# Performance work log

Hardware: AMD Instinct MI355X
Metric: run time of the kernel (lower is better)

Reference implementation:

```python
import jax, jax.numpy as jnp
import numpy as np

HEAD_SIZE = 128  # matches init head_size; original scales by global head_size**-0.5


def setup_inputs() -> dict:
    key = jax.random.key(0)
    k1, k2, k3, k4 = jax.random.split(key, 4)
    B, T, C, D = 16, 2048, 1024, HEAD_SIZE
    x = jax.random.normal(k1, (B, T, C), dtype=jnp.float32)
    # torch Linear weight is [out,in]; store transposed so forward is x @ W
    Wq = jax.random.normal(k2, (C, D), dtype=jnp.float32) * (C ** -0.5)
    Wk = jax.random.normal(k3, (C, D), dtype=jnp.float32) * (C ** -0.5)
    Wv = jax.random.normal(k4, (C, D), dtype=jnp.float32) * (C ** -0.5)
    return {"x": x, "Wq": Wq, "Wk": Wk, "Wv": Wv}


def reference(x, Wq, Wk, Wv):
    # x: [B,T,C]; projections -> [B,T,D]
    q = x @ Wq
    k = x @ Wk
    v = x @ Wv
    T = x.shape[1]
    scale = HEAD_SIZE ** -0.5
    # scores: [B,T,T]
    wei = jnp.einsum("btd,bsd->bts", q, k) * scale
    causal = jnp.tril(jnp.ones((T, T), dtype=bool))  # tril buffer
    wei = jnp.where(causal, wei, -jnp.inf)
    wei = jax.nn.softmax(wei, axis=-1)
    # dropout is identity in eval mode (deterministic reference)
    return wei @ v  # [B,T,D]
```

## Files before the change

### kernel.cpp

```cpp
#include <hip/hip_runtime.h>
#include <hip/hip_bf16.h>

typedef short bf16x8 __attribute__((ext_vector_type(8)));
typedef float f32x4 __attribute__((ext_vector_type(4)));
typedef unsigned short u16x4 __attribute__((ext_vector_type(4)));

#define B_ 16
#define T_ 2048
#define C_ 1024
#define D_ 128
#define M_ (B_ * T_)

static __device__ __forceinline__ unsigned short f2bf(float f) {
    unsigned int u = __builtin_bit_cast(unsigned int, f);
    unsigned int r = (u + 0x7fffu + ((u >> 16) & 1u)) >> 16;
    return (unsigned short)r;
}

static __device__ __forceinline__ void gll16(const unsigned short* g, unsigned short* l) {
    __builtin_amdgcn_global_load_lds(
        (const __attribute__((address_space(1))) void*)g,
        (__attribute__((address_space(3))) void*)l, 16, 0, 0);
}

__global__ void cvt_kernel(const float* __restrict__ x, unsigned short* __restrict__ xb) {
    int idx = blockIdx.x * 256 + threadIdx.x;
#pragma unroll
    for (int it = 0; it < 4; ++it, idx += 1048576) {
        const int row = idx >> 7;
        const int g   = idx & 127;
        const int gs  = (g & ~7) | ((g & 7) ^ (row & 7));
        const float* src = x + (size_t)row * C_ + g * 8;
        float4 v0 = *(const float4*)src;
        float4 v1 = *(const float4*)(src + 4);
        bf16x8 h;
        h[0] = (short)f2bf(v0.x); h[1] = (short)f2bf(v0.y);
        h[2] = (short)f2bf(v0.z); h[3] = (short)f2bf(v0.w);
        h[4] = (short)f2bf(v1.x); h[5] = (short)f2bf(v1.y);
        h[6] = (short)f2bf(v1.z); h[7] = (short)f2bf(v1.w);
        *(bf16x8*)&xb[(size_t)row * C_ + gs * 8] = h;
    }
}

#define TPAD 133

__global__ void wt_kernel(const float* __restrict__ Wq, const float* __restrict__ Wk,
                          const float* __restrict__ Wv, unsigned short* __restrict__ Wt) {
    __shared__ float Tl[64 * TPAD];
    const int o  = blockIdx.x >> 4;
    const int k0 = (blockIdx.x & 15) * 64;
    const float* W = (o == 0) ? Wq : (o == 1) ? Wk : Wv;
    const int tid = threadIdx.x;

    const int kr = tid >> 5;
    const int n4 = (tid & 31) * 4;
#pragma unroll
    for (int j = 0; j < 8; ++j) {
        float4 v = *(const float4*)(W + (size_t)(k0 + kr + j * 8) * 128 + n4);
        *(float4*)&Tl[(kr + j * 8) * TPAD + n4] = v;
    }
    __syncthreads();

    const int nb = tid >> 3;
    const int kg = (tid & 7) * 8;
#pragma unroll
    for (int j = 0; j < 4; ++j) {
        const int nn = nb + j * 32;
        const int kk = kg ^ ((nn & 7) * 8);
        bf16x8 v;
#pragma unroll
        for (int e = 0; e < 8; ++e)
            v[e] = (short)f2bf(Tl[(kk + e) * TPAD + nn]);
        *(bf16x8*)&Wt[((size_t)o * 128 + nn) * 1024 + k0 + kg] = v;
    }
}

__launch_bounds__(256, 3)
__global__ void qkv_kernel(const unsigned short* __restrict__ xb, const unsigned short* __restrict__ Wt,
                           unsigned short* __restrict__ Q, unsigned short* __restrict__ K,
                           unsigned short* __restrict__ Vt) {
    __shared__ unsigned short Alds[128 * 64];
    __shared__ unsigned short Blds[128 * 64];

    const int tid  = threadIdx.x;
    const int lane = tid & 63;
    const int w    = tid >> 6;
    const int wr   = w >> 1;
    const int wc   = w & 1;
    const int lr   = lane & 15;
    const int lk   = lane >> 4;

    const int nt = blockIdx.x >> 8;
    const int mt = blockIdx.x & 255;
    const int m0 = mt * 128;
    const int n0 = nt * 128;

    const int srow = tid >> 3;
    const int sg   = (tid & 7) * 8;

    f32x4 acc[4][4] = {};

    for (int t = 0; t < 16; ++t) {
        const int k0 = t * 64;
#pragma unroll
        for (int j = 0; j < 4; ++j) {
            gll16(xb + (size_t)(m0 + j * 32 + srow) * C_ + k0 + sg,
                  &Alds[(j * 32 + w * 8) * 64]);
            gll16(Wt + (size_t)(n0 + j * 32 + srow) * C_ + k0 + sg,
                  &Blds[(j * 32 + w * 8) * 64]);
        }
        __syncthreads();

#pragma unroll
        for (int kk = 0; kk < 2; ++kk) {
            bf16x8 a[4], b[4];
#pragma unroll
            for (int rb = 0; rb < 4; ++rb) {
                const int row = wr * 64 + rb * 16 + lr;
                a[rb] = *(bf16x8*)&Alds[row * 64 + ((kk * 32 + lk * 8) ^ ((row & 7) * 8))];
            }
#pragma unroll
            for (int nb = 0; nb < 4; ++nb) {
                const int row = wc * 64 + nb * 16 + lr;
                b[nb] = *(bf16x8*)&Blds[row * 64 + ((kk * 32 + lk * 8) ^ ((row & 7) * 8))];
            }
#pragma unroll
            for (int rb = 0; rb < 4; ++rb)
#pragma unroll
                for (int nb = 0; nb < 4; ++nb)
                    acc[rb][nb] = __builtin_amdgcn_mfma_f32_16x16x32_bf16(a[rb], b[nb], acc[rb][nb], 0, 0, 0);
        }
        __syncthreads();
    }

    const float qscale = 0.08838834764831845f;
    const int b  = m0 / T_;
    const int t0 = m0 % T_;
#pragma unroll
    for (int rb = 0; rb < 4; ++rb) {
#pragma unroll
        for (int nb = 0; nb < 4; ++nb) {
            const int row0 = wr * 64 + rb * 16 + lk * 4;
            const int d    = wc * 64 + nb * 16 + lr;
            f32x4 a = acc[rb][nb];
            if (nt == 0) {
#pragma unroll
                for (int r = 0; r < 4; ++r)
                    Q[(size_t)(m0 + row0 + r) * D_ + d] = f2bf(a[r] * qscale);
            } else if (nt == 1) {
#pragma unroll
                for (int r = 0; r < 4; ++r)
                    K[(size_t)(m0 + row0 + r) * D_ + d] = f2bf(a[r]);
            } else {
                u16x4 pv;
#pragma unroll
                for (int r = 0; r < 4; ++r) pv[r] = f2bf(a[r]);
                *(u16x4*)&Vt[((size_t)b * D_ + d) * T_ + t0 + row0] = pv;
            }
        }
    }
}

#define KSTR 132
#define VSTR 68
#define PSTR 68

__launch_bounds__(256, 2)
__global__ void attn_kernel(const unsigned short* __restrict__ Q, const unsigned short* __restrict__ K,
                            const unsigned short* __restrict__ Vt, float* __restrict__ out) {
    __shared__ unsigned short Klds[2][64 * KSTR];
    __shared__ unsigned short Vlds[2][128 * VSTR];
    __shared__ unsigned short Plds[4][16 * PSTR];

    const int tid  = threadIdx.x;
    const int lane = tid & 63;
    const int w    = tid >> 6;
    const int lr   = lane & 15;
    const int lk   = lane >> 4;

    int bid = blockIdx.x;
    int batch, qt;
    if (bid < 256) { batch = bid >> 4; qt = bid & 15; }
    else           { bid -= 256; batch = bid >> 4; qt = 31 - (bid & 15); }

    const unsigned short* Qb = Q  + (size_t)batch * T_ * D_;
    const unsigned short* Kb = K  + (size_t)batch * T_ * D_;
    const unsigned short* Vb = Vt + (size_t)batch * D_ * T_;
    float* outb = out + (size_t)batch * T_ * D_;

    const int kxr = tid >> 4;
    const int kxc = (tid & 15) * 8;
    const int vxr = tid >> 3;
    const int vxc = (tid & 7) * 8;

    bf16x8 kr[4], vr[4];
    auto kv_load = [&](int kvt) {
        const int kv0 = kvt * 64;
#pragma unroll
        for (int j = 0; j < 4; ++j)
            kr[j] = *(const bf16x8*)(Kb + (size_t)(kv0 + kxr + j * 16) * D_ + kxc);
#pragma unroll
        for (int j = 0; j < 4; ++j)
            vr[j] = *(const bf16x8*)(Vb + (size_t)(vxr + j * 32) * T_ + kv0 + vxc);
    };
    auto kv_write = [&](int buf) {
#pragma unroll
        for (int j = 0; j < 4; ++j)
            *(bf16x8*)&Klds[buf][(kxr + j * 16) * KSTR + kxc] = kr[j];
#pragma unroll
        for (int j = 0; j < 4; ++j)
            *(bf16x8*)&Vlds[buf][(vxr + j * 32) * VSTR + vxc] = vr[j];
    };

    const int qw = qt * 64 + w * 16;

    bf16x8 qf[4];
#pragma unroll
    for (int c = 0; c < 4; ++c)
        qf[c] = *(const bf16x8*)(Qb + (size_t)(qw + lr) * D_ + lk * 8 + c * 32);

    f32x4 o_acc[8] = {};
    float mrun[4] = {-1e30f, -1e30f, -1e30f, -1e30f};
    float lrun[4] = {0.f, 0.f, 0.f, 0.f};

    kv_load(0);
    kv_write(0);

    for (int kvt = 0; kvt <= qt; ++kvt) {
        const int cur = kvt & 1;
        __syncthreads();
        if (kvt < qt) kv_load(kvt + 1);

        f32x4 s[4];
#pragma unroll
        for (int nb = 0; nb < 4; ++nb) {
            f32x4 a = {};
#pragma unroll
            for (int c = 0; c < 4; ++c) {
                bf16x8 kf = *(bf16x8*)&Klds[cur][(nb * 16 + lr) * KSTR + lk * 8 + c * 32];
                a = __builtin_amdgcn_mfma_f32_16x16x32_bf16(qf[c], kf, a, 0, 0, 0);
            }
            s[nb] = a;
        }

        if (kvt == qt) {
#pragma unroll
            for (int nb = 0; nb < 4; ++nb)
#pragma unroll
                for (int r = 0; r < 4; ++r) {
                    int qg = qw + lk * 4 + r;
                    int kg = kvt * 64 + nb * 16 + lr;
                    if (kg > qg) s[nb][r] = -1e30f;
                }
        }

        float scale_[4];
#pragma unroll
        for (int r = 0; r < 4; ++r) {
            float mx = fmaxf(fmaxf(s[0][r], s[1][r]), fmaxf(s[2][r], s[3][r]));
            mx = fmaxf(mx, __shfl_xor(mx, 1));
            mx = fmaxf(mx, __shfl_xor(mx, 2));
            mx = fmaxf(mx, __shfl_xor(mx, 4));
            mx = fmaxf(mx, __shfl_xor(mx, 8));
            float mnew = fmaxf(mrun[r], mx);
            scale_[r]  = __expf(mrun[r] - mnew);
            mrun[r]    = mnew;
            lrun[r]   *= scale_[r];
        }
#pragma unroll
        for (int db = 0; db < 8; ++db)
#pragma unroll
            for (int r = 0; r < 4; ++r) o_acc[db][r] *= scale_[r];

#pragma unroll
        for (int nb = 0; nb < 4; ++nb)
#pragma unroll
            for (int r = 0; r < 4; ++r) {
                float p = __expf(s[nb][r] - mrun[r]);
                lrun[r] += p;
                Plds[w][(lk * 4 + r) * PSTR + nb * 16 + lr] = f2bf(p);
            }
        asm volatile("s_waitcnt lgkmcnt(0)" ::: "memory");
        __builtin_amdgcn_sched_barrier(0);

        bf16x8 pa[2];
#pragma unroll
        for (int c = 0; c < 2; ++c)
            pa[c] = *(bf16x8*)&Plds[w][lr * PSTR + lk * 8 + c * 32];
#pragma unroll
        for (int db = 0; db < 8; ++db) {
            f32x4 oo = o_acc[db];
#pragma unroll
            for (int c = 0; c < 2; ++c) {
                bf16x8 vf = *(bf16x8*)&Vlds[cur][(db * 16 + lr) * VSTR + lk * 8 + c * 32];
                oo = __builtin_amdgcn_mfma_f32_16x16x32_bf16(pa[c], vf, oo, 0, 0, 0);
            }
            o_acc[db] = oo;
        }

        if (kvt < qt) kv_write(cur ^ 1);
    }

#pragma unroll
    for (int r = 0; r < 4; ++r) {
        float sgm = lrun[r];
        sgm += __shfl_xor(sgm, 1);
        sgm += __shfl_xor(sgm, 2);
        sgm += __shfl_xor(sgm, 4);
        sgm += __shfl_xor(sgm, 8);
        lrun[r] = 1.0f / sgm;
    }
#pragma unroll
    for (int db = 0; db < 8; ++db)
#pragma unroll
        for (int r = 0; r < 4; ++r)
            outb[(size_t)(qw + lk * 4 + r) * D_ + db * 16 + lr] = o_acc[db][r] * lrun[r];
}

extern "C" void kernel_launch(void* const* d_in, const int* in_sizes, int n_in,
                              void* d_out, int out_size, void* d_ws, size_t ws_size,
                              hipStream_t stream) {
    const float* x  = (const float*)d_in[0];
    const float* Wq = (const float*)d_in[1];
    const float* Wk = (const float*)d_in[2];
    const float* Wv = (const float*)d_in[3];

    unsigned short* xb  = (unsigned short*)d_ws;
    unsigned short* Wt  = (unsigned short*)((char*)d_ws + (64u << 20));
    unsigned short* Qw  = (unsigned short*)((char*)d_ws + (65u << 20));
    unsigned short* Kw  = Qw + (size_t)M_ * D_;
    unsigned short* Vtw = Kw + (size_t)M_ * D_;

    hipLaunchKernelGGL(cvt_kernel, dim3(4096), dim3(256), 0, stream, x, xb);
    hipLaunchKernelGGL(wt_kernel, dim3(48), dim3(256), 0, stream, Wq, Wk, Wv, Wt);
    hipLaunchKernelGGL(qkv_kernel, dim3(768), dim3(256), 0, stream, xb, Wt, Qw, Kw, Vtw);
    hipLaunchKernelGGL(attn_kernel, dim3(512), dim3(256), 0, stream, Qw, Kw, Vtw, (float*)d_out);
}
```

Measured before the change: 118.7 us.

## Fuse fp32-to-bf16 conversion into QKV GEMM with double buffering, remap attention blocks

Drops the separate x conversion kernel. The QKV GEMM now loads fp32 x straight into registers, converts it to bf16 and writes it to double-buffered LDS, while weight tiles are prefetched asynchronously one step ahead. This removes the 64MB bf16 write and reread of x, at the cost of three times as many x reads overall (three N tiles each read the fp32 rows), more registers, and occupancy lowered from 3 to 2. The attention block index mapping also changes so that blocks sharing a batch land on the same XCD, with causal tiles paired for load balance.

Result: slower. 134.7 us (+13.5%).

```diff
diff --git a/kernel.cpp b/kernel.cpp
--- a/kernel.cpp
+++ b/kernel.cpp
@@ -21,25 +21,6 @@
     __builtin_amdgcn_global_load_lds(
         (const __attribute__((address_space(1))) void*)g,
         (__attribute__((address_space(3))) void*)l, 16, 0, 0);
-}
-
-__global__ void cvt_kernel(const float* __restrict__ x, unsigned short* __restrict__ xb) {
-    int idx = blockIdx.x * 256 + threadIdx.x;
-#pragma unroll
-    for (int it = 0; it < 4; ++it, idx += 1048576) {
-        const int row = idx >> 7;
-        const int g   = idx & 127;
-        const int gs  = (g & ~7) | ((g & 7) ^ (row & 7));
-        const float* src = x + (size_t)row * C_ + g * 8;
-        float4 v0 = *(const float4*)src;
-        float4 v1 = *(const float4*)(src + 4);
-        bf16x8 h;
-        h[0] = (short)f2bf(v0.x); h[1] = (short)f2bf(v0.y);
-        h[2] = (short)f2bf(v0.z); h[3] = (short)f2bf(v0.w);
-        h[4] = (short)f2bf(v1.x); h[5] = (short)f2bf(v1.y);
-        h[6] = (short)f2bf(v1.z); h[7] = (short)f2bf(v1.w);
-        *(bf16x8*)&xb[(size_t)row * C_ + gs * 8] = h;
-    }
 }
 
 #define TPAD 133
@@ -75,12 +56,14 @@
     }
 }
 
-__launch_bounds__(256, 3)
-__global__ void qkv_kernel(const unsigned short* __restrict__ xb, const unsigned short* __restrict__ Wt,
+__launch_bounds__(256, 2)
+__global__ void qkv_kernel(const float* __restrict__ x, const unsigned short* __restrict__ Wt,
                            unsigned short* __restrict__ Q, unsigned short* __restrict__ K,
                            unsigned short* __restrict__ Vt) {
-    __shared__ unsigned short Alds[128 * 64];
-    __shared__ unsigned short Blds[128 * 64];
+    __shared__ unsigned short A0[128 * 64];
+    __shared__ unsigned short A1[128 * 64];
+    __shared__ unsigned short B0[128 * 64];
+    __shared__ unsigned short B1[128 * 64];
 
     const int tid  = threadIdx.x;
     const int lane = tid & 63;
@@ -98,31 +81,51 @@
     const int srow = tid >> 3;
     const int sg   = (tid & 7) * 8;
 
+    auto stageB = [&](unsigned short* Bl, int t) {
+        const int k0 = t * 64;
+#pragma unroll
+        for (int j = 0; j < 4; ++j)
+            gll16(Wt + (size_t)(n0 + j * 32 + srow) * C_ + k0 + sg,
+                  &Bl[(j * 32 + w * 8) * 64]);
+    };
+
+    const int axr = tid >> 4;
+    const int axc = (tid & 15) * 4;
+    float4 ar[8];
+    auto loadA = [&](int k0) {
+#pragma unroll
+        for (int j = 0; j < 8; ++j)
+            ar[j] = *(const float4*)(x + (size_t)(m0 + axr + j * 16) * C_ + k0 + axc);
+    };
+    const int awcol = ((((axc >> 3) ^ (axr & 7)) << 3) | (axc & 7));
+    auto writeA = [&](unsigned short* Al) {
+#pragma unroll
+        for (int j = 0; j < 8; ++j) {
+            const int row = axr + j * 16;
+            const int col = ((((axc >> 3) ^ (row & 7)) << 3) | (axc & 7));
+            u16x4 v;
+            v[0] = f2bf(ar[j].x); v[1] = f2bf(ar[j].y);
+            v[2] = f2bf(ar[j].z); v[3] = f2bf(ar[j].w);
+            *(u16x4*)&Al[row * 64 + col] = v;
+        }
+    };
+    (void)awcol;
+
     f32x4 acc[4][4] = {};
 
-    for (int t = 0; t < 16; ++t) {
-        const int k0 = t * 64;
-#pragma unroll
-        for (int j = 0; j < 4; ++j) {
-            gll16(xb + (size_t)(m0 + j * 32 + srow) * C_ + k0 + sg,
-                  &Alds[(j * 32 + w * 8) * 64]);
-            gll16(Wt + (size_t)(n0 + j * 32 + srow) * C_ + k0 + sg,
-                  &Blds[(j * 32 + w * 8) * 64]);
-        }
-        __syncthreads();
-
+    auto compute = [&](const unsigned short* Al, const unsigned short* Bl) {
 #pragma unroll
         for (int kk = 0; kk < 2; ++kk) {
             bf16x8 a[4], b[4];
 #pragma unroll
             for (int rb = 0; rb < 4; ++rb) {
                 const int row = wr * 64 + rb * 16 + lr;
-                a[rb] = *(bf16x8*)&Alds[row * 64 + ((kk * 32 + lk * 8) ^ ((row & 7) * 8))];
+                a[rb] = *(const bf16x8*)&Al[row * 64 + ((kk * 32 + lk * 8) ^ ((row & 7) * 8))];
             }
 #pragma unroll
             for (int nb = 0; nb < 4; ++nb) {
                 const int row = wc * 64 + nb * 16 + lr;
-                b[nb] = *(bf16x8*)&Blds[row * 64 + ((kk * 32 + lk * 8) ^ ((row & 7) * 8))];
+                b[nb] = *(const bf16x8*)&Bl[row * 64 + ((kk * 32 + lk * 8) ^ ((row & 7) * 8))];
             }
 #pragma unroll
             for (int rb = 0; rb < 4; ++rb)
@@ -130,6 +133,24 @@
                 for (int nb = 0; nb < 4; ++nb)
                     acc[rb][nb] = __builtin_amdgcn_mfma_f32_16x16x32_bf16(a[rb], b[nb], acc[rb][nb], 0, 0, 0);
         }
+    };
+
+    loadA(0);
+    stageB(B0, 0);
+    writeA(A0);
+    __syncthreads();
+
+    for (int ts = 0; ts < 8; ++ts) {
+        const int t = ts * 2;
+        loadA((t + 1) * 64);
+        stageB(B1, t + 1);
+        compute(A0, B0);
+        writeA(A1);
+        __syncthreads();
+
+        if (ts < 7) { loadA((t + 2) * 64); stageB(B0, t + 2); }
+        compute(A1, B1);
+        if (ts < 7) writeA(A0);
         __syncthreads();
     }
 
@@ -178,10 +199,11 @@
     const int lr   = lane & 15;
     const int lk   = lane >> 4;
 
-    int bid = blockIdx.x;
-    int batch, qt;
-    if (bid < 256) { batch = bid >> 4; qt = bid & 15; }
-    else           { bid -= 256; batch = bid >> 4; qt = 31 - (bid & 15); }
+    const int xcd = blockIdx.x & 7;
+    const int p   = blockIdx.x >> 3;
+    const int batch = xcd * 2 + (p & 1);
+    const int q     = p >> 1;
+    const int qt    = (q < 16) ? q : (47 - q);
 
     const unsigned short* Qb = Q  + (size_t)batch * T_ * D_;
     const unsigned short* Kb = K  + (size_t)batch * T_ * D_;
@@ -276,9 +298,9 @@
         for (int nb = 0; nb < 4; ++nb)
 #pragma unroll
             for (int r = 0; r < 4; ++r) {
-                float p = __expf(s[nb][r] - mrun[r]);
-                lrun[r] += p;
-                Plds[w][(lk * 4 + r) * PSTR + nb * 16 + lr] = f2bf(p);
+                float p_ = __expf(s[nb][r] - mrun[r]);
+                lrun[r] += p_;
+                Plds[w][(lk * 4 + r) * PSTR + nb * 16 + lr] = f2bf(p_);
             }
         asm volatile("s_waitcnt lgkmcnt(0)" ::: "memory");
         __builtin_amdgcn_sched_barrier(0);
@@ -325,14 +347,12 @@
     const float* Wk = (const float*)d_in[2];
     const float* Wv = (const float*)d_in[3];
 
-    unsigned short* xb  = (unsigned short*)d_ws;
-    unsigned short* Wt  = (unsigned short*)((char*)d_ws + (64u << 20));
-    unsigned short* Qw  = (unsigned short*)((char*)d_ws + (65u << 20));
+    unsigned short* Wt  = (unsigned short*)d_ws;
+    unsigned short* Qw  = (unsigned short*)((char*)d_ws + (1 << 20));
     unsigned short* Kw  = Qw + (size_t)M_ * D_;
     unsigned short* Vtw = Kw + (size_t)M_ * D_;
 
-    hipLaunchKernelGGL(cvt_kernel, dim3(4096), dim3(256), 0, stream, x, xb);
     hipLaunchKernelGGL(wt_kernel, dim3(48), dim3(256), 0, stream, Wq, Wk, Wv, Wt);
-    hipLaunchKernelGGL(qkv_kernel, dim3(768), dim3(256), 0, stream, xb, Wt, Qw, Kw, Vtw);
+    hipLaunchKernelGGL(qkv_kernel, dim3(768), dim3(256), 0, stream, x, Wt, Qw, Kw, Vtw);
     hipLaunchKernelGGL(attn_kernel, dim3(512), dim3(256), 0, stream, Qw, Kw, Vtw, (float*)d_out);
 }
```
